# Optimization experiments

Hardware: AMD Instinct MI355X
Metric: run time of the kernel (lower is better)

## Reference

```python
import math
import jax, jax.numpy as jnp
import numpy as np
from jax.scipy.special import erf

SIGMA = 0.5  # RegLoss sigma
N, C, D = 1048576, 10, 64


def setup_inputs() -> dict:
    key = jax.random.key(0)
    k1, k2, k3 = jax.random.split(key, 3)
    yhat = jax.random.randint(k1, (N,), 0, C)
    yg = jax.random.normal(k2, (N, C), dtype=jnp.float32)
    u_zg = jax.random.normal(k3, (N, D), dtype=jnp.float32)
    lmbd = jnp.float32(0.1)
    return {"yhat": yhat, "yg": yg, "u_zg": u_zg, "lmbd": lmbd}


def reference(yhat, yg, u_zg, lmbd):
    K = yg.shape[-1]          # classes; yhat values index this axis
    Dg = u_zg.shape[-1]
    inv = 1.0 / (SIGMA * math.sqrt(2.0))
    # elementwise erf regularizer, summed per row: f(u) = 0.5 - 0.5*erf((-1/2 - u)/(sigma*sqrt(2)))
    row_reg = jnp.sum(0.5 - 0.5 * erf((-0.5 - u_zg) * inv), axis=-1)      # [N]
    # per-row cross entropy with target = its own cluster id (unique-class loop collapses to this)
    row_ce = jax.nn.logsumexp(yg, axis=-1) - jnp.take_along_axis(yg, yhat[:, None], axis=-1)[:, 0]  # [N]
    ones = jnp.ones_like(row_ce)
    counts = jax.ops.segment_sum(ones, yhat, num_segments=K)              # [K]
    seg_reg = jax.ops.segment_sum(row_reg, yhat, num_segments=K)
    seg_ce = jax.ops.segment_sum(row_ce, yhat, num_segments=K)
    present = counts > 0
    denom = jnp.where(present, counts, 1.0)
    reg_c = seg_reg / (denom * Dg)   # mean over N_c * D elements per class
    aux_c = seg_ce / denom           # mean CE per class
    n_unique = jnp.sum(present.astype(jnp.float32))
    reg_loss = jnp.sum(jnp.where(present, reg_c, 0.0)) / n_unique
    aux_loss = jnp.sum(jnp.where(present, aux_c, 0.0)) / n_unique
    return aux_loss + lmbd * reg_loss
```

## Files before the change

### kernel.cpp

```cpp
#include <hip/hip_runtime.h>
#include <math.h>

#define N_ROWS 1048576
#define C_CLS 10
#define D_DIM 64
#define NBLK 2048
#define NTHR 256
#define NWAVES (NBLK * NTHR / 64)

typedef float v4f __attribute__((ext_vector_type(4)));

__device__ __forceinline__ float f_reg(float u) {
    float z  = fmaf(2.0f, u, 1.0f);
    float z2 = z * z;
    float a  = z * fmaf(0.1017966f, z2, 2.3048496f);
    float e  = __builtin_amdgcn_exp2f(-a);
    return __builtin_amdgcn_rcpf(1.0f + e);
}

__device__ __forceinline__ float red16(float t) {
    t += __shfl_xor(t, 1);
    t += __shfl_xor(t, 2);
    t += __shfl_xor(t, 4);
    t += __shfl_xor(t, 8);
    return t;
}

__device__ __forceinline__ v4f nt_load_f4(const float* p) {
    return __builtin_nontemporal_load((const v4f*)p);
}

__global__ __launch_bounds__(256) void aux_main(
    const int* __restrict__ yhat,
    const float* __restrict__ yg,
    const float* __restrict__ u_zg,
    float* __restrict__ ws)
{
    __shared__ float s_reg[C_CLS];
    __shared__ float s_ce[C_CLS];
    __shared__ float s_cnt[C_CLS];
    __shared__ float s_yg[NTHR / 64][64 * 11];
    const int tid = threadIdx.x;
    if (tid < C_CLS) { s_reg[tid] = 0.f; s_ce[tid] = 0.f; s_cnt[tid] = 0.f; }
    __syncthreads();

    const int gtid = blockIdx.x * NTHR + tid;
    const int lane = tid & 63;
    const int wv = tid >> 6;
    const int gwave = gtid >> 6;
    const int NG = N_ROWS / 4;
    const int sub = lane >> 4;

    int g = gwave;
    for (; g + 3 * NWAVES < NG; g += 4 * NWAVES) {
        const int g1 = g + NWAVES, g2 = g + 2 * NWAVES, g3 = g + 3 * NWAVES;
        v4f v0 = nt_load_f4(u_zg + ((size_t)g  * 64 + lane) * 4);
        v4f v1 = nt_load_f4(u_zg + ((size_t)g1 * 64 + lane) * 4);
        v4f v2 = nt_load_f4(u_zg + ((size_t)g2 * 64 + lane) * 4);
        v4f v3 = nt_load_f4(u_zg + ((size_t)g3 * 64 + lane) * 4);
        int c0 = yhat[g  * 4 + sub];
        int c1 = yhat[g1 * 4 + sub];
        int c2 = yhat[g2 * 4 + sub];
        int c3 = yhat[g3 * 4 + sub];
        float t0 = f_reg(v0.x) + f_reg(v0.y) + f_reg(v0.z) + f_reg(v0.w);
        float t1 = f_reg(v1.x) + f_reg(v1.y) + f_reg(v1.z) + f_reg(v1.w);
        float t2 = f_reg(v2.x) + f_reg(v2.y) + f_reg(v2.z) + f_reg(v2.w);
        float t3 = f_reg(v3.x) + f_reg(v3.y) + f_reg(v3.z) + f_reg(v3.w);
        t0 = red16(t0); t1 = red16(t1); t2 = red16(t2); t3 = red16(t3);
        if ((lane & 15) == 0) {
            atomicAdd(&s_reg[c0], t0);
            atomicAdd(&s_reg[c1], t1);
            atomicAdd(&s_reg[c2], t2);
            atomicAdd(&s_reg[c3], t3);
        }
    }
    for (; g < NG; g += NWAVES) {
        v4f v = nt_load_f4(u_zg + ((size_t)g * 64 + lane) * 4);
        int c = yhat[g * 4 + sub];
        float t = f_reg(v.x) + f_reg(v.y) + f_reg(v.z) + f_reg(v.w);
        t = red16(t);
        if ((lane & 15) == 0) atomicAdd(&s_reg[c], t);
    }

    {
        const int NCHUNK = N_ROWS / 64;
        float* __restrict__ myw = s_yg[wv];
        for (int chunk = gwave; chunk < NCHUNK; chunk += NWAVES) {
            const float* __restrict__ cb = yg + (size_t)chunk * 640;
#pragma unroll
            for (int k = 0; k < 5; ++k) {
                float2 r = *(const float2*)(cb + k * 128 + 2 * lane);
                int f0 = k * 128 + 2 * lane;
                int r0 = f0 / 10;
                int c0 = f0 - r0 * 10;
                myw[r0 * 11 + c0]     = r.x;
                myw[r0 * 11 + c0 + 1] = r.y;
            }
            const float* __restrict__ my = &myw[lane * 11];
            float y0 = my[0], y1 = my[1], y2 = my[2], y3 = my[3], y4 = my[4];
            float y5 = my[5], y6 = my[6], y7 = my[7], y8 = my[8], y9 = my[9];
            int row = chunk * 64 + lane;
            int c = yhat[row];
            float m = fmaxf(fmaxf(fmaxf(y0, y1), fmaxf(y2, y3)),
                     fmaxf(fmaxf(fmaxf(y4, y5), fmaxf(y6, y7)),
                           fmaxf(y8, y9)));
            float s = __expf(y0 - m) + __expf(y1 - m)
                    + __expf(y2 - m) + __expf(y3 - m)
                    + __expf(y4 - m) + __expf(y5 - m)
                    + __expf(y6 - m) + __expf(y7 - m)
                    + __expf(y8 - m) + __expf(y9 - m);
            float ce = m + __logf(s) - my[c];
            atomicAdd(&s_ce[c], ce);
            atomicAdd(&s_cnt[c], 1.0f);
        }
    }

    __syncthreads();
    if (tid < 3 * C_CLS) {
        float v = (tid < C_CLS) ? s_reg[tid]
                : (tid < 2 * C_CLS) ? s_ce[tid - C_CLS]
                : s_cnt[tid - 2 * C_CLS];
        ws[(size_t)tid * NBLK + blockIdx.x] = v;
    }
}

__global__ __launch_bounds__(1024) void aux_final(
    const float* __restrict__ ws,
    const float* __restrict__ lmbd,
    float* __restrict__ out)
{
    __shared__ double s_tot[32];
    const int tid = threadIdx.x;
    const int lane = tid & 63;
    const int wave = tid >> 6;

    for (int e = wave; e < 3 * C_CLS; e += 16) {
        const float4* p = (const float4*)(ws + (size_t)e * NBLK);
        double acc = 0.0;
#pragma unroll
        for (int i = 0; i < 8; ++i) {
            float4 v = p[lane + 64 * i];
            acc += (double)v.x + (double)v.y + (double)v.z + (double)v.w;
        }
        for (int off = 32; off > 0; off >>= 1)
            acc += __shfl_xor(acc, off);
        if (lane == 0) s_tot[e] = acc;
    }
    __syncthreads();
    if (tid == 0) {
        double sreg = 0.0, sce = 0.0, nu = 0.0;
        for (int k = 0; k < C_CLS; ++k) {
            double cnt = s_tot[2 * C_CLS + k];
            if (cnt > 0.0) {
                sreg += s_tot[k] / (cnt * (double)D_DIM);
                sce  += s_tot[C_CLS + k] / cnt;
                nu += 1.0;
            }
        }
        out[0] = (float)(sce / nu + (double)lmbd[0] * (sreg / nu));
    }
}

extern "C" void kernel_launch(void* const* d_in, const int* in_sizes, int n_in,
                              void* d_out, int out_size, void* d_ws, size_t ws_size,
                              hipStream_t stream) {
    const int*   yhat = (const int*)d_in[0];
    const float* yg   = (const float*)d_in[1];
    const float* u_zg = (const float*)d_in[2];
    const float* lmbd = (const float*)d_in[3];
    float* out = (float*)d_out;
    float* ws  = (float*)d_ws;

    aux_main<<<NBLK, NTHR, 0, stream>>>(yhat, yg, u_zg, ws);
    aux_final<<<1, 1024, 0, stream>>>(ws, lmbd, out);
}
```

Measured before the change: 68.46 us.

## Interleave cross-entropy chunks into reg loop with fixed trip counts and plain loads

Replaces the generic strided loops with a fixed 8-iteration loop over u_zg groups (NG/(4*NWAVES)=8) and inserts one yg cross-entropy chunk mid-loop plus one after it, since each wave handles exactly two chunks. The intent is to overlap the yg phase with the u_zg streaming and remove loop tail and bound checks. It also switches the u_zg loads from nontemporal to ordinary float4 loads. The trip counts are now hardcoded to the fixed problem size.

```diff
diff --git a/kernel.cpp b/kernel.cpp
--- a/kernel.cpp
+++ b/kernel.cpp
@@ -7,8 +7,6 @@
 #define NBLK 2048
 #define NTHR 256
 #define NWAVES (NBLK * NTHR / 64)
-
-typedef float v4f __attribute__((ext_vector_type(4)));
 
 __device__ __forceinline__ float f_reg(float u) {
     float z  = fmaf(2.0f, u, 1.0f);
@@ -26,10 +24,6 @@
     return t;
 }
 
-__device__ __forceinline__ v4f nt_load_f4(const float* p) {
-    return __builtin_nontemporal_load((const v4f*)p);
-}
-
 __global__ __launch_bounds__(256) void aux_main(
     const int* __restrict__ yhat,
     const float* __restrict__ yg,
@@ -44,20 +38,50 @@
     if (tid < C_CLS) { s_reg[tid] = 0.f; s_ce[tid] = 0.f; s_cnt[tid] = 0.f; }
     __syncthreads();
 
-    const int gtid = blockIdx.x * NTHR + tid;
     const int lane = tid & 63;
     const int wv = tid >> 6;
-    const int gwave = gtid >> 6;
-    const int NG = N_ROWS / 4;
+    const int gwave = blockIdx.x * (NTHR / 64) + wv;
     const int sub = lane >> 4;
+    const float4* __restrict__ u4 = (const float4*)u_zg;
+    float* __restrict__ myw = s_yg[wv];
+
+    auto do_chunk = [&](int chunk) {
+        const float* __restrict__ cb = yg + (size_t)chunk * 640;
+#pragma unroll
+        for (int k = 0; k < 5; ++k) {
+            float2 r = *(const float2*)(cb + k * 128 + 2 * lane);
+            int f0 = k * 128 + 2 * lane;
+            int r0 = f0 / 10;
+            int c0 = f0 - r0 * 10;
+            myw[r0 * 11 + c0]     = r.x;
+            myw[r0 * 11 + c0 + 1] = r.y;
+        }
+        const float* __restrict__ my = &myw[lane * 11];
+        float y0 = my[0], y1 = my[1], y2 = my[2], y3 = my[3], y4 = my[4];
+        float y5 = my[5], y6 = my[6], y7 = my[7], y8 = my[8], y9 = my[9];
+        int row = chunk * 64 + lane;
+        int c = yhat[row];
+        float m = fmaxf(fmaxf(fmaxf(y0, y1), fmaxf(y2, y3)),
+                 fmaxf(fmaxf(fmaxf(y4, y5), fmaxf(y6, y7)),
+                       fmaxf(y8, y9)));
+        float s = __expf(y0 - m) + __expf(y1 - m)
+                + __expf(y2 - m) + __expf(y3 - m)
+                + __expf(y4 - m) + __expf(y5 - m)
+                + __expf(y6 - m) + __expf(y7 - m)
+                + __expf(y8 - m) + __expf(y9 - m);
+        float ce = m + __logf(s) - my[c];
+        atomicAdd(&s_ce[c], ce);
+        atomicAdd(&s_cnt[c], 1.0f);
+    };
 
     int g = gwave;
-    for (; g + 3 * NWAVES < NG; g += 4 * NWAVES) {
+#pragma unroll 1
+    for (int it = 0; it < 8; ++it, g += 4 * NWAVES) {
         const int g1 = g + NWAVES, g2 = g + 2 * NWAVES, g3 = g + 3 * NWAVES;
-        v4f v0 = nt_load_f4(u_zg + ((size_t)g  * 64 + lane) * 4);
-        v4f v1 = nt_load_f4(u_zg + ((size_t)g1 * 64 + lane) * 4);
-        v4f v2 = nt_load_f4(u_zg + ((size_t)g2 * 64 + lane) * 4);
-        v4f v3 = nt_load_f4(u_zg + ((size_t)g3 * 64 + lane) * 4);
+        float4 v0 = u4[(size_t)g  * 64 + lane];
+        float4 v1 = u4[(size_t)g1 * 64 + lane];
+        float4 v2 = u4[(size_t)g2 * 64 + lane];
+        float4 v3 = u4[(size_t)g3 * 64 + lane];
         int c0 = yhat[g  * 4 + sub];
         int c1 = yhat[g1 * 4 + sub];
         int c2 = yhat[g2 * 4 + sub];
@@ -73,47 +97,9 @@
             atomicAdd(&s_reg[c2], t2);
             atomicAdd(&s_reg[c3], t3);
         }
+        if (it == 3) do_chunk(gwave);
     }
-    for (; g < NG; g += NWAVES) {
-        v4f v = nt_load_f4(u_zg + ((size_t)g * 64 + lane) * 4);
-        int c = yhat[g * 4 + sub];
-        float t = f_reg(v.x) + f_reg(v.y) + f_reg(v.z) + f_reg(v.w);
-        t = red16(t);
-        if ((lane & 15) == 0) atomicAdd(&s_reg[c], t);
-    }
-
-    {
-        const int NCHUNK = N_ROWS / 64;
-        float* __restrict__ myw = s_yg[wv];
-        for (int chunk = gwave; chunk < NCHUNK; chunk += NWAVES) {
-            const float* __restrict__ cb = yg + (size_t)chunk * 640;
-#pragma unroll
-            for (int k = 0; k < 5; ++k) {
-                float2 r = *(const float2*)(cb + k * 128 + 2 * lane);
-                int f0 = k * 128 + 2 * lane;
-                int r0 = f0 / 10;
-                int c0 = f0 - r0 * 10;
-                myw[r0 * 11 + c0]     = r.x;
-                myw[r0 * 11 + c0 + 1] = r.y;
-            }
-            const float* __restrict__ my = &myw[lane * 11];
-            float y0 = my[0], y1 = my[1], y2 = my[2], y3 = my[3], y4 = my[4];
-            float y5 = my[5], y6 = my[6], y7 = my[7], y8 = my[8], y9 = my[9];
-            int row = chunk * 64 + lane;
-            int c = yhat[row];
-            float m = fmaxf(fmaxf(fmaxf(y0, y1), fmaxf(y2, y3)),
-                     fmaxf(fmaxf(fmaxf(y4, y5), fmaxf(y6, y7)),
-                           fmaxf(y8, y9)));
-            float s = __expf(y0 - m) + __expf(y1 - m)
-                    + __expf(y2 - m) + __expf(y3 - m)
-                    + __expf(y4 - m) + __expf(y5 - m)
-                    + __expf(y6 - m) + __expf(y7 - m)
-                    + __expf(y8 - m) + __expf(y9 - m);
-            float ce = m + __logf(s) - my[c];
-            atomicAdd(&s_ce[c], ce);
-            atomicAdd(&s_cnt[c], 1.0f);
-        }
-    }
+    do_chunk(gwave + NWAVES);
 
     __syncthreads();
     if (tid < 3 * C_CLS) {
```

After: 67.58 us. About the same (-1.3%).
